# Optimization experiments

Measured on AMD Instinct MI355X. Metric: run time of the kernel, lower is better.

The kernel has to match this reference:

```python
import jax, jax.numpy as jnp
import numpy as np

N_NODES = 100000
N_EDGES = 1600000
IN_CH = 128
OUT_CH = 32
HEADS = 2
NEG_SLOPE = 0.2  # GATv2Conv default negative_slope


def setup_inputs() -> dict:
    key = jax.random.key(0)
    ks = jax.random.split(key, 6)
    x = jax.random.normal(ks[0], (N_NODES, IN_CH), dtype=jnp.float32)
    edge_index = jax.random.randint(ks[1], (2, N_EDGES), 0, N_NODES, dtype=jnp.int64)
    s_in = 1.0 / np.sqrt(IN_CH)
    Wl = jax.random.normal(ks[2], (IN_CH, HEADS * OUT_CH), dtype=jnp.float32) * s_in  # lin_l weight
    Wr = jax.random.normal(ks[3], (IN_CH, HEADS * OUT_CH), dtype=jnp.float32) * s_in  # lin_r weight
    bl = jnp.zeros((HEADS * OUT_CH,), dtype=jnp.float32)
    br = jnp.zeros((HEADS * OUT_CH,), dtype=jnp.float32)
    att = jax.random.normal(ks[4], (HEADS, OUT_CH), dtype=jnp.float32) * (1.0 / np.sqrt(OUT_CH))
    bias = jnp.zeros((OUT_CH,), dtype=jnp.float32)  # output bias (concat=False -> size out_channels)
    return {"x": x, "Wl": Wl, "bl": bl, "Wr": Wr, "br": br, "att": att, "bias": bias,
            "edge_index": edge_index}


def _gatv2_layer(x, Wl, bl, Wr, br, att, bias, edge_index):
    N = x.shape[0]
    H, C = att.shape
    # add self loops (GATv2Conv default add_self_loops=True)
    loops = jnp.arange(N, dtype=edge_index.dtype)
    src = jnp.concatenate([edge_index[0], loops])  # [E+N] message sources j
    dst = jnp.concatenate([edge_index[1], loops])  # [E+N] message targets i
    # per-node linear transforms (share_weights=False)
    xl = (x @ Wl + bl).reshape(N, H, C)
    xr = (x @ Wr + br).reshape(N, H, C)
    # GATv2 dynamic attention: a^T LeakyReLU(xl[j] + xr[i])
    h = xl[src] + xr[dst]                                   # [E, H, C]
    e = jnp.einsum('ehc,hc->eh', jax.nn.leaky_relu(h, NEG_SLOPE), att)  # [E, H]
    # segment softmax over incoming edges of each target node
    m = jax.ops.segment_max(e, dst, num_segments=N)         # [N, H]
    a = jnp.exp(e - m[dst])
    denom = jax.ops.segment_sum(a, dst, num_segments=N)     # [N, H]
    alpha = a / (denom[dst] + 1e-16)                        # [E, H]
    # weighted scatter-add of source messages
    out = jax.ops.segment_sum(alpha[:, :, None] * xl[src], dst, num_segments=N)  # [N, H, C]
    out = out.mean(axis=1) + bias                           # concat=False -> head mean
    return jax.nn.silu(out)                                 # activation='silu'


def reference(x, Wl, bl, Wr, br, att, bias, edge_index):
    return _gatv2_layer(x, Wl, bl, Wr, br, att, bias, edge_index)
```

## Files before the change

### kernel.cpp

```cpp
#include <hip/hip_runtime.h>
#include <math.h>

#define BSH 9
#define BMASK ((1 << BSH) - 1)
#define CAP 12288
#define ACH 2048

typedef unsigned int uint;
typedef __attribute__((ext_vector_type(8))) short bf16x8;
typedef __attribute__((ext_vector_type(4))) float f32x4;
typedef __attribute__((ext_vector_type(2))) float f32x2;

static __device__ __forceinline__ unsigned short f2bf(float f) {
    uint u = __float_as_uint(f);
    return (unsigned short)((u + 0x7fffu + ((u >> 16) & 1u)) >> 16);
}

static __device__ __forceinline__ f32x2 dec2(uint u) {
    f32x2 r;
    r.x = __uint_as_float(u << 16);
    r.y = __uint_as_float(u & 0xffff0000u);
    return r;
}

static __device__ __forceinline__ f32x2 abs2(f32x2 h) {
    f32x2 r;
    r.x = __uint_as_float(__float_as_uint(h.x) & 0x7fffffffu);
    r.y = __uint_as_float(__float_as_uint(h.y) & 0x7fffffffu);
    return r;
}

static __device__ __forceinline__ float qsum(float p) {
    p += __uint_as_float(__builtin_amdgcn_mov_dpp(__float_as_uint(p), 0xB1, 0xF, 0xF, true));
    p += __uint_as_float(__builtin_amdgcn_mov_dpp(__float_as_uint(p), 0x4E, 0xF, 0xF, true));
    return p;
}

__global__ __launch_bounds__(256) void k_init(int* __restrict__ bcur, int NB) {
    int i = blockIdx.x * 256 + threadIdx.x;
    if (i < NB) bcur[i] = i * CAP;
}

static __device__ __forceinline__ void gemm_body(char* smem,
        const float* __restrict__ x,
        const float* __restrict__ Wl, const float* __restrict__ bl,
        const float* __restrict__ Wr, const float* __restrict__ br,
        unsigned short* __restrict__ xlh, float* __restrict__ xr, int N, int bid)
{
    char* sA = smem;
    char* sB = smem + 32768;
    const int t = threadIdx.x;
    const int base = bid * 128;

#pragma unroll 4
    for (int s = 0; s < 16; ++s) {
        int f = s * 256 + t;
        int r = f >> 5;
        int c4 = f & 31;
        int rg = base + r; if (rg >= N) rg = N - 1;
        float4 v = ((const float4*)x)[(size_t)rg * 32 + c4];
        uint2 pk;
        pk.x = (uint)f2bf(v.x) | ((uint)f2bf(v.y) << 16);
        pk.y = (uint)f2bf(v.z) | ((uint)f2bf(v.w) << 16);
        int kb = c4 * 8;
        *(uint2*)(sA + r * 256 + (kb ^ ((r & 7) << 4))) = pk;
    }
#pragma unroll
    for (int s = 0; s < 8; ++s) {
        int tau = s * 256 + t;
        int m  = tau >> 10;
        int k2 = (tau >> 4) & 63;
        int n4 = tau & 15;
        const float4* Wp = (const float4*)(m ? Wr : Wl);
        float4 a = Wp[(2 * k2) * 16 + n4];
        float4 b = Wp[(2 * k2 + 1) * 16 + n4];
        const float* af = (const float*)&a;
        const float* bf = (const float*)&b;
#pragma unroll
        for (int j = 0; j < 4; ++j) {
            int n = m * 64 + n4 * 4 + j;
            uint u = (uint)f2bf(af[j]) | ((uint)f2bf(bf[j]) << 16);
            *(uint*)(sB + n * 256 + ((k2 * 4) ^ ((n & 7) << 4))) = u;
        }
    }
    __syncthreads();

    const int w = t >> 6;
    const int lo = t & 15;
    const int hi = (t & 63) >> 4;
    f32x4 acc[2][8];
#pragma unroll
    for (int f = 0; f < 2; ++f)
#pragma unroll
        for (int j = 0; j < 8; ++j)
            acc[f][j] = (f32x4){0.f, 0.f, 0.f, 0.f};

#pragma unroll
    for (int ks = 0; ks < 4; ++ks) {
        int kb = ks * 64 + hi * 16;
        bf16x8 av[2], bv[8];
#pragma unroll
        for (int f = 0; f < 2; ++f) {
            int r = w * 32 + f * 16 + lo;
            av[f] = *(const bf16x8*)(sA + r * 256 + (kb ^ ((r & 7) << 4)));
        }
#pragma unroll
        for (int j = 0; j < 8; ++j) {
            int nn = j * 16 + lo;
            bv[j] = *(const bf16x8*)(sB + nn * 256 + (kb ^ ((nn & 7) << 4)));
        }
#pragma unroll
        for (int f = 0; f < 2; ++f)
#pragma unroll
            for (int j = 0; j < 8; ++j)
                acc[f][j] = __builtin_amdgcn_mfma_f32_16x16x32_bf16(av[f], bv[j], acc[f][j], 0, 0, 0);
    }

#pragma unroll
    for (int f = 0; f < 2; ++f) {
        int rbase = base + w * 32 + f * 16 + hi * 4;
#pragma unroll
        for (int j = 0; j < 8; ++j) {
            int nn = j * 16 + lo;
            float bvv = (j < 4) ? bl[nn] : br[nn - 64];
            float vv[4] = {acc[f][j][0] + bvv, acc[f][j][1] + bvv,
                           acc[f][j][2] + bvv, acc[f][j][3] + bvv};
            if (j < 4) {
#pragma unroll
                for (int q = 0; q < 4; ++q)
                    if (rbase + q < N) xlh[(size_t)(rbase + q) * 64 + nn] = f2bf(vv[q]);
            } else {
#pragma unroll
                for (int q = 0; q < 4; ++q)
                    if (rbase + q < N) xr[(size_t)(rbase + q) * 64 + (nn - 64)] = vv[q];
            }
        }
    }
}

static __device__ __forceinline__ void scatA_body(char* smem,
        const int* __restrict__ ei, int* __restrict__ bcur,
        unsigned* __restrict__ pairs, int E, int T, int NB, int bid)
{
    int* h = (int*)smem;
    int* basem = h + 256;
    int b0 = bid * ACH;
    int cnt = min(ACH, T - b0);
    h[threadIdx.x] = 0;
    __syncthreads();
    for (int i = threadIdx.x; i < cnt; i += 256) {
        int t = b0 + i;
        int d = (t < E) ? ei[E + t] : (t - E);
        atomicAdd(&h[d >> BSH], 1);
    }
    __syncthreads();
    if (threadIdx.x < NB) {
        int c = h[threadIdx.x];
        basem[threadIdx.x] = c ? atomicAdd(&bcur[threadIdx.x], c) : 0;
    }
    __syncthreads();
    h[threadIdx.x] = 0;
    __syncthreads();
    for (int i = threadIdx.x; i < cnt; i += 256) {
        int t = b0 + i;
        int s, d;
        if (t < E) { s = ei[t]; d = ei[E + t]; } else { s = t - E; d = s; }
        int b = d >> BSH;
        int idx = atomicAdd(&h[b], 1);
        pairs[basem[b] + idx] = ((unsigned)s << BSH) | (unsigned)(d & BMASK);
    }
}

__global__ __launch_bounds__(256) void k_gs(const float* __restrict__ x,
        const float* __restrict__ Wl, const float* __restrict__ bl,
        const float* __restrict__ Wr, const float* __restrict__ br,
        unsigned short* __restrict__ xlh, float* __restrict__ xr, int N,
        const int* __restrict__ ei, int* __restrict__ bcur,
        unsigned* __restrict__ pairs, int E, int T, int NB, int GB)
{
    extern __shared__ char smem[];
    if ((int)blockIdx.x < GB)
        gemm_body(smem, x, Wl, bl, Wr, br, xlh, xr, N, blockIdx.x);
    else
        scatA_body(smem, ei, bcur, pairs, E, T, NB, blockIdx.x - GB);
}

__global__ __launch_bounds__(512) void k_scatB(const unsigned* __restrict__ pairs,
                                               const int* __restrict__ bcur,
                                               int* __restrict__ src_s, int2* __restrict__ rowrng, int N) {
    __shared__ int cnt[512];
    __shared__ int sm[512];
    __shared__ int lofs[512];
    int b = blockIdx.x;
    int beg = b * CAP, end = bcur[b];
    int nbase = b << BSH;
    cnt[threadIdx.x] = 0;
    __syncthreads();
    for (int i = beg + threadIdx.x; i < end; i += 512)
        atomicAdd(&cnt[pairs[i] & BMASK], 1);
    __syncthreads();
    int v = cnt[threadIdx.x];
    sm[threadIdx.x] = v;
    __syncthreads();
    int acc = v;
    for (int off = 1; off < 512; off <<= 1) {
        int t = (threadIdx.x >= off) ? sm[threadIdx.x - off] : 0;
        __syncthreads();
        acc += t;
        sm[threadIdx.x] = acc;
        __syncthreads();
    }
    int excl = acc - v;
    lofs[threadIdx.x] = excl;
    int n = nbase + threadIdx.x;
    if (n < N) rowrng[n] = make_int2(beg + excl, beg + excl + v);
    cnt[threadIdx.x] = 0;
    __syncthreads();
    for (int i = beg + threadIdx.x; i < end; i += 512) {
        unsigned p = pairs[i];
        int dl = p & BMASK;
        int idx = atomicAdd(&cnt[dl], 1);
        src_s[beg + lofs[dl] + idx] = p >> BSH;
    }
}

__global__ __launch_bounds__(256) void k_fused(const int2* __restrict__ rowrng,
        const int* __restrict__ src_s, const unsigned short* __restrict__ xlh,
        const float* __restrict__ xr, const float* __restrict__ att,
        const float* __restrict__ bias, float* __restrict__ out, int N)
{
    int n = blockIdx.x * 32 + (threadIdx.x >> 3);
    int j = threadIdx.x & 7;
    if (n >= N) return;
    const uint4* xl4 = (const uint4*)xlh + j;
    f32x2 xr2[4], a06[4], a04[4];
    {
        float4 a = ((const float4*)xr)[(size_t)n * 16 + j * 2];
        float4 b = ((const float4*)xr)[(size_t)n * 16 + j * 2 + 1];
        xr2[0] = (f32x2){a.x, a.y}; xr2[1] = (f32x2){a.z, a.w};
        xr2[2] = (f32x2){b.x, b.y}; xr2[3] = (f32x2){b.z, b.w};
        float4 c = ((const float4*)att)[j * 2];
        float4 d = ((const float4*)att)[j * 2 + 1];
        a06[0] = (f32x2){0.6f * c.x, 0.6f * c.y}; a06[1] = (f32x2){0.6f * c.z, 0.6f * c.w};
        a06[2] = (f32x2){0.6f * d.x, 0.6f * d.y}; a06[3] = (f32x2){0.6f * d.z, 0.6f * d.w};
        a04[0] = (f32x2){0.4f * c.x, 0.4f * c.y}; a04[1] = (f32x2){0.4f * c.z, 0.4f * c.w};
        a04[2] = (f32x2){0.4f * d.x, 0.4f * d.y}; a04[3] = (f32x2){0.4f * d.z, 0.4f * d.w};
    }
    int2 rr = rowrng[n];
    float ssum = 0.f;
    f32x2 acc2[4] = {(f32x2){0.f,0.f}, (f32x2){0.f,0.f}, (f32x2){0.f,0.f}, (f32x2){0.f,0.f}};

#define EDGE_BODY(u)                                                      \
    {                                                                     \
        f32x2 v0 = dec2((u).x), v1 = dec2((u).y), v2 = dec2((u).z), v3 = dec2((u).w); \
        f32x2 h0 = v0 + xr2[0], h1 = v1 + xr2[1], h2 = v2 + xr2[2], h3 = v3 + xr2[3]; \
        f32x2 pa = h0 * a06[0]; pa += h1 * a06[1]; pa += h2 * a06[2]; pa += h3 * a06[3]; \
        pa += abs2(h0) * a04[0]; pa += abs2(h1) * a04[1];                 \
        pa += abs2(h2) * a04[2]; pa += abs2(h3) * a04[3];                 \
        float p = pa.x + pa.y;                                            \
        p = qsum(p);                                                      \
        float wq = __expf(p);                                             \
        ssum += wq;                                                       \
        f32x2 ws = (f32x2){wq, wq};                                       \
        acc2[0] += ws * v0; acc2[1] += ws * v1;                           \
        acc2[2] += ws * v2; acc2[3] += ws * v3;                           \
    }

    int i = rr.x;
    for (; i + 8 <= rr.y; i += 8) {
        uint4 u[8];
#pragma unroll
        for (int q = 0; q < 8; ++q)
            u[q] = xl4[((uint)src_s[i + q] << 3)];
#pragma unroll
        for (int q = 0; q < 8; ++q)
            EDGE_BODY(u[q]);
    }
    if (i + 4 <= rr.y) {
        uint4 u[4];
#pragma unroll
        for (int q = 0; q < 4; ++q)
            u[q] = xl4[((uint)src_s[i + q] << 3)];
#pragma unroll
        for (int q = 0; q < 4; ++q)
            EDGE_BODY(u[q]);
        i += 4;
    }
    for (; i < rr.y; ++i) {
        uint4 u0 = xl4[((uint)src_s[i] << 3)];
        EDGE_BODY(u0);
    }
#undef EDGE_BODY

    float inv = 1.f / ssum;
    float o[8];
#pragma unroll
    for (int q = 0; q < 4; ++q) {
        float vx = acc2[q].x * inv, vy = acc2[q].y * inv;
        o[2 * q]     = (vx + __shfl_xor(vx, 4)) * 0.5f;
        o[2 * q + 1] = (vy + __shfl_xor(vy, 4)) * 0.5f;
    }
    if (j < 4) {
        float4 b0 = ((const float4*)bias)[j * 2];
        float4 b1 = ((const float4*)bias)[j * 2 + 1];
        float4 r0, r1;
        r0.x = o[0] + b0.x; r0.y = o[1] + b0.y; r0.z = o[2] + b0.z; r0.w = o[3] + b0.w;
        r1.x = o[4] + b1.x; r1.y = o[5] + b1.y; r1.z = o[6] + b1.z; r1.w = o[7] + b1.w;
        r0.x = r0.x / (1.f + __expf(-r0.x));
        r0.y = r0.y / (1.f + __expf(-r0.y));
        r0.z = r0.z / (1.f + __expf(-r0.z));
        r0.w = r0.w / (1.f + __expf(-r0.w));
        r1.x = r1.x / (1.f + __expf(-r1.x));
        r1.y = r1.y / (1.f + __expf(-r1.y));
        r1.z = r1.z / (1.f + __expf(-r1.z));
        r1.w = r1.w / (1.f + __expf(-r1.w));
        ((float4*)out)[(size_t)n * 8 + j * 2] = r0;
        ((float4*)out)[(size_t)n * 8 + j * 2 + 1] = r1;
    }
}

extern "C" void kernel_launch(void* const* d_in, const int* in_sizes, int n_in,
                              void* d_out, int out_size, void* d_ws, size_t ws_size,
                              hipStream_t stream) {
    const float* x    = (const float*)d_in[0];
    const float* Wl   = (const float*)d_in[1];
    const float* bl   = (const float*)d_in[2];
    const float* Wr   = (const float*)d_in[3];
    const float* br   = (const float*)d_in[4];
    const float* att  = (const float*)d_in[5];
    const float* bias = (const float*)d_in[6];
    const int*   ei   = (const int*)d_in[7];
    float* out = (float*)d_out;

    const int N = in_sizes[0] / 128;
    const int E = in_sizes[7] / 2;
    const int T = E + N;
    const int NB = (N + (1 << BSH) - 1) >> BSH;

    char* p = (char*)d_ws;
    auto take = [&](size_t bytes) {
        char* r = p;
        p += (bytes + 255) & ~(size_t)255;
        return r;
    };
    unsigned short* xlh = (unsigned short*)take((size_t)N * 64 * 2);
    float*    xr     = (float*)take((size_t)N * 64 * 4);
    unsigned* pairs  = (unsigned*)take((size_t)NB * CAP * 4);
    int*      src_s  = (int*)take((size_t)NB * CAP * 4);
    int2*     rowrng = (int2*)take((size_t)N * 8);
    int*      bcur   = (int*)take((size_t)NB * 4);

    const int GB = (N + 127) / 128;
    const int SB = (T + ACH - 1) / ACH;
    k_init <<<1,           256, 0, stream>>>(bcur, NB);
    k_gs   <<<GB + SB,     256, 65536, stream>>>(x, Wl, bl, Wr, br, xlh, xr, N,
                                                 ei, bcur, pairs, E, T, NB, GB);
    k_scatB<<<NB,          512, 0, stream>>>(pairs, bcur, src_s, rowrng, N);
    k_fused<<<(N + 31) / 32, 256, 0, stream>>>(rowrng, src_s, xlh, xr, att, bias, out, N);
}
```

Baseline: 111.6 us.

## Load GEMM A operand directly from global, halve LDS, replace init kernel with memset

The GEMM no longer stages x through shared memory. Each lane loads its two float4s per k-step straight from global and packs them to bf16 with v_cvt_pk_bf16_f32, which halves dynamic LDS to 32KB. With launch_bounds(256,4) this is meant to allow more resident blocks. The bucket cursor now counts from zero, so the k_init kernel is replaced by a memset and the CAP offset is added at use. The B swizzle changes to a 16-way XOR. The trade-off is that global loads move into the MFMA loop, giving less coalescing for A, and there is some risk the memset launch costs as much as the kernel it replaces.

```diff
diff --git a/kernel.cpp b/kernel.cpp
--- a/kernel.cpp
+++ b/kernel.cpp
@@ -14,6 +14,16 @@
 static __device__ __forceinline__ unsigned short f2bf(float f) {
     uint u = __float_as_uint(f);
     return (unsigned short)((u + 0x7fffu + ((u >> 16) & 1u)) >> 16);
+}
+
+static __device__ __forceinline__ bf16x8 pack8(float4 a, float4 b) {
+    uint p0, p1, p2, p3;
+    asm("v_cvt_pk_bf16_f32 %0, %1, %2" : "=v"(p0) : "v"(a.x), "v"(a.y));
+    asm("v_cvt_pk_bf16_f32 %0, %1, %2" : "=v"(p1) : "v"(a.z), "v"(a.w));
+    asm("v_cvt_pk_bf16_f32 %0, %1, %2" : "=v"(p2) : "v"(b.x), "v"(b.y));
+    asm("v_cvt_pk_bf16_f32 %0, %1, %2" : "=v"(p3) : "v"(b.z), "v"(b.w));
+    uint4 u = make_uint4(p0, p1, p2, p3);
+    return *(bf16x8*)&u;
 }
 
 static __device__ __forceinline__ f32x2 dec2(uint u) {
@@ -36,35 +46,15 @@
     return p;
 }
 
-__global__ __launch_bounds__(256) void k_init(int* __restrict__ bcur, int NB) {
-    int i = blockIdx.x * 256 + threadIdx.x;
-    if (i < NB) bcur[i] = i * CAP;
-}
-
-static __device__ __forceinline__ void gemm_body(char* smem,
+static __device__ __forceinline__ void gemm_body(char* sB,
         const float* __restrict__ x,
         const float* __restrict__ Wl, const float* __restrict__ bl,
         const float* __restrict__ Wr, const float* __restrict__ br,
         unsigned short* __restrict__ xlh, float* __restrict__ xr, int N, int bid)
 {
-    char* sA = smem;
-    char* sB = smem + 32768;
     const int t = threadIdx.x;
     const int base = bid * 128;
 
-#pragma unroll 4
-    for (int s = 0; s < 16; ++s) {
-        int f = s * 256 + t;
-        int r = f >> 5;
-        int c4 = f & 31;
-        int rg = base + r; if (rg >= N) rg = N - 1;
-        float4 v = ((const float4*)x)[(size_t)rg * 32 + c4];
-        uint2 pk;
-        pk.x = (uint)f2bf(v.x) | ((uint)f2bf(v.y) << 16);
-        pk.y = (uint)f2bf(v.z) | ((uint)f2bf(v.w) << 16);
-        int kb = c4 * 8;
-        *(uint2*)(sA + r * 256 + (kb ^ ((r & 7) << 4))) = pk;
-    }
 #pragma unroll
     for (int s = 0; s < 8; ++s) {
         int tau = s * 256 + t;
@@ -80,7 +70,7 @@
         for (int j = 0; j < 4; ++j) {
             int n = m * 64 + n4 * 4 + j;
             uint u = (uint)f2bf(af[j]) | ((uint)f2bf(bf[j]) << 16);
-            *(uint*)(sB + n * 256 + ((k2 * 4) ^ ((n & 7) << 4))) = u;
+            *(uint*)(sB + n * 256 + ((k2 * 4) ^ ((n & 15) << 4))) = u;
         }
     }
     __syncthreads();
@@ -88,6 +78,11 @@
     const int w = t >> 6;
     const int lo = t & 15;
     const int hi = (t & 63) >> 4;
+    int row0 = base + w * 32 + lo;
+    int row1 = row0 + 16;
+    const float4* x40 = (const float4*)x + (size_t)(row0 < N ? row0 : N - 1) * 32;
+    const float4* x41 = (const float4*)x + (size_t)(row1 < N ? row1 : N - 1) * 32;
+
     f32x4 acc[2][8];
 #pragma unroll
     for (int f = 0; f < 2; ++f)
@@ -98,16 +93,14 @@
 #pragma unroll
     for (int ks = 0; ks < 4; ++ks) {
         int kb = ks * 64 + hi * 16;
+        int f4 = ks * 8 + hi * 2;
         bf16x8 av[2], bv[8];
-#pragma unroll
-        for (int f = 0; f < 2; ++f) {
-            int r = w * 32 + f * 16 + lo;
-            av[f] = *(const bf16x8*)(sA + r * 256 + (kb ^ ((r & 7) << 4)));
-        }
+        av[0] = pack8(x40[f4], x40[f4 + 1]);
+        av[1] = pack8(x41[f4], x41[f4 + 1]);
 #pragma unroll
         for (int j = 0; j < 8; ++j) {
             int nn = j * 16 + lo;
-            bv[j] = *(const bf16x8*)(sB + nn * 256 + (kb ^ ((nn & 7) << 4)));
+            bv[j] = *(const bf16x8*)(sB + nn * 256 + (kb ^ ((nn & 15) << 4)));
         }
 #pragma unroll
         for (int f = 0; f < 2; ++f)
@@ -156,7 +149,7 @@
     __syncthreads();
     if (threadIdx.x < NB) {
         int c = h[threadIdx.x];
-        basem[threadIdx.x] = c ? atomicAdd(&bcur[threadIdx.x], c) : 0;
+        basem[threadIdx.x] = c ? (threadIdx.x * CAP + atomicAdd(&bcur[threadIdx.x], c)) : 0;
     }
     __syncthreads();
     h[threadIdx.x] = 0;
@@ -171,7 +164,7 @@
     }
 }
 
-__global__ __launch_bounds__(256) void k_gs(const float* __restrict__ x,
+__global__ __launch_bounds__(256, 4) void k_gs(const float* __restrict__ x,
         const float* __restrict__ Wl, const float* __restrict__ bl,
         const float* __restrict__ Wr, const float* __restrict__ br,
         unsigned short* __restrict__ xlh, float* __restrict__ xr, int N,
@@ -192,7 +185,7 @@
     __shared__ int sm[512];
     __shared__ int lofs[512];
     int b = blockIdx.x;
-    int beg = b * CAP, end = bcur[b];
+    int beg = b * CAP, end = beg + bcur[b];
     int nbase = b << BSH;
     cnt[threadIdx.x] = 0;
     __syncthreads();
@@ -352,9 +345,9 @@
 
     const int GB = (N + 127) / 128;
     const int SB = (T + ACH - 1) / ACH;
-    k_init <<<1,           256, 0, stream>>>(bcur, NB);
-    k_gs   <<<GB + SB,     256, 65536, stream>>>(x, Wl, bl, Wr, br, xlh, xr, N,
-                                                 ei, bcur, pairs, E, T, NB, GB);
-    k_scatB<<<NB,          512, 0, stream>>>(pairs, bcur, src_s, rowrng, N);
+    hipMemsetAsync(bcur, 0, (size_t)NB * 4, stream);
+    k_gs   <<<GB + SB,       256, 32768, stream>>>(x, Wl, bl, Wr, br, xlh, xr, N,
+                                                   ei, bcur, pairs, E, T, NB, GB);
+    k_scatB<<<NB,            512, 0, stream>>>(pairs, bcur, src_s, rowrng, N);
     k_fused<<<(N + 31) / 32, 256, 0, stream>>>(rowrng, src_s, xlh, xr, att, bias, out, N);
 }
```

Result: faster. 103.9 us (-6.8%).
